# Kernel optimization log

Measured on AMD Instinct MI355X. Metric: run time of the kernel, lower is better.

Reference implementation:

```python
import jax, jax.numpy as jnp
import numpy as np

SEQ_LEN = 4096
IN_DIM = 1024
QVK_DIM = 1024


def setup_inputs() -> dict:
    key = jax.random.key(0)
    kx, kw = jax.random.split(key)
    x = jax.random.normal(kx, (SEQ_LEN, IN_DIM), dtype=jnp.float32)
    # glorot-uniform-ish scale for W: limit = sqrt(6/(fan_in+fan_out))
    limit = np.sqrt(6.0 / (IN_DIM + 3 * QVK_DIM)).astype(np.float32)
    W = jax.random.uniform(kw, (IN_DIM, 3 * QVK_DIM), dtype=jnp.float32,
                           minval=-limit, maxval=limit)
    return {"x": x, "W": W}


def reference(x, W):
    seq_len = x.shape[0]
    qvk = x @ W                                   # [S, 3*D]
    # NOTE: original splits as queries, VALS, keys (vals is the middle chunk)
    queries, vals, keys = jnp.split(qvk, 3, axis=1)
    raw = (queries @ keys.T) / jnp.sqrt(jnp.float32(QVK_DIM))  # [S, S]
    # causal mask: strictly-upper-triangular entries -> -inf (same as the
    # original's scatter of -inf at triu_indices(seq_len, 1))
    causal = jnp.tril(jnp.ones((seq_len, seq_len), dtype=bool))
    raw = jnp.where(causal, raw, -jnp.inf)
    weights = jax.nn.softmax(raw, axis=1)
    return weights @ vals                         # [S, D]
```

## Files before the change

kernel.cpp:

```cpp
#include <hip/hip_runtime.h>

#define SEQ 4096
#define KDIM 1024
#define NQKV 3072
#define BK 32

typedef __bf16 bf16x8 __attribute__((ext_vector_type(8)));
typedef float  f32x4  __attribute__((ext_vector_type(4)));

__device__ __forceinline__ unsigned short f2b(float f) {
    unsigned int u = __float_as_uint(f);
    u += 0x7FFFu + ((u >> 16) & 1u);
    return (unsigned short)(u >> 16);
}
__device__ __forceinline__ float b2f(unsigned short h) {
    return __uint_as_float(((unsigned int)h) << 16);
}

__device__ __forceinline__ void gld_lds16(const unsigned short* g, unsigned short* l) {
    __builtin_amdgcn_global_load_lds(
        (const __attribute__((address_space(1))) void*)g,
        (__attribute__((address_space(3))) void*)l, 16, 0, 0);
}

__device__ __forceinline__ void stage_tiles(
    const unsigned short* Ag, int lda, const unsigned short* Bg, int ldb,
    int k0, unsigned short* sA, unsigned short* sB, int wave, int lane)
{
    #pragma unroll
    for (int i = 0; i < 2; ++i) {
        int c = wave * 128 + i * 64 + lane;
        int row = c >> 2, slot = c & 3;
        int p = slot ^ ((row >> 1) & 3);
        gld_lds16(Ag + row * lda + k0 + p * 8, sA + (wave * 2 + i) * 512);
        gld_lds16(Bg + row * ldb + k0 + p * 8, sB + (wave * 2 + i) * 512);
    }
}

__device__ __forceinline__ const unsigned short* frag_addr(
    const unsigned short* s, int row, int quad)
{
    return s + row * 32 + (quad ^ ((row >> 1) & 3)) * 8;
}

__device__ __forceinline__ void compute_tile(
    const unsigned short* sA, const unsigned short* sB, f32x4 acc[4][4],
    int wm, int wn, int lr, int quad)
{
    bf16x8 af[4], bq[4];
    #pragma unroll
    for (int i = 0; i < 4; ++i)
        af[i] = *(const bf16x8*)frag_addr(sA, wm + 16 * i + lr, quad);
    #pragma unroll
    for (int j = 0; j < 4; ++j)
        bq[j] = *(const bf16x8*)frag_addr(sB, wn + 16 * j + lr, quad);
    #pragma unroll
    for (int i = 0; i < 4; ++i)
        #pragma unroll
        for (int j = 0; j < 4; ++j)
            acc[i][j] = __builtin_amdgcn_mfma_f32_16x16x32_bf16(af[i], bq[j], acc[i][j], 0, 0, 0);
}

__device__ __forceinline__ void mfma_db(
    const unsigned short* Ag, int lda, const unsigned short* Bg, int ldb,
    int kLen, unsigned short* lds, f32x4 acc[4][4])
{
    const int tid  = threadIdx.x;
    const int wave = tid >> 6, lane = tid & 63;
    const int lr   = lane & 15, quad = lane >> 4;
    const int wm   = (wave >> 1) * 64, wn = (wave & 1) * 64;
    unsigned short* sA0 = lds;
    unsigned short* sB0 = lds + 4096;
    unsigned short* sA1 = lds + 8192;
    unsigned short* sB1 = lds + 12288;

    stage_tiles(Ag, lda, Bg, ldb, 0, sA0, sB0, wave, lane);
    int k = BK;
    #pragma unroll 1
    for (; k + BK < kLen; k += 2 * BK) {
        __syncthreads();
        stage_tiles(Ag, lda, Bg, ldb, k, sA1, sB1, wave, lane);
        compute_tile(sA0, sB0, acc, wm, wn, lr, quad);
        __syncthreads();
        stage_tiles(Ag, lda, Bg, ldb, k + BK, sA0, sB0, wave, lane);
        compute_tile(sA1, sB1, acc, wm, wn, lr, quad);
    }
    if (k < kLen) {
        __syncthreads();
        stage_tiles(Ag, lda, Bg, ldb, k, sA1, sB1, wave, lane);
        compute_tile(sA0, sB0, acc, wm, wn, lr, quad);
        __syncthreads();
        compute_tile(sA1, sB1, acc, wm, wn, lr, quad);
    } else {
        __syncthreads();
        compute_tile(sA0, sB0, acc, wm, wn, lr, quad);
    }
}

__device__ __forceinline__ void zero_acc(f32x4 acc[4][4]) {
    const f32x4 z = {0.f, 0.f, 0.f, 0.f};
    #pragma unroll
    for (int i = 0; i < 4; ++i)
        #pragma unroll
        for (int j = 0; j < 4; ++j) acc[i][j] = z;
}

__device__ __forceinline__ void store_rows_bf16(
    f32x4 acc[4][4], unsigned short* Cw, int ld, unsigned short* lw, int lane)
{
    const int lr = lane & 15, quad = lane >> 4;
    #pragma unroll
    for (int i = 0; i < 4; ++i) {
        #pragma unroll
        for (int j = 0; j < 4; ++j)
            #pragma unroll
            for (int r = 0; r < 4; ++r)
                lw[(quad * 4 + r) * 72 + j * 16 + lr] = f2b(acc[i][j][r]);
        #pragma unroll
        for (int t = 0; t < 2; ++t) {
            int chunk = t * 64 + lane;
            int rl = chunk >> 3, c8 = chunk & 7;
            uint4 v = *(const uint4*)(lw + rl * 72 + c8 * 8);
            *(uint4*)(Cw + (16 * i + rl) * ld + c8 * 8) = v;
        }
    }
}

__device__ __forceinline__ void store_cols_bf16(
    f32x4 acc[4][4], unsigned short* Vw, unsigned short* lw, int lane)
{
    const int lr = lane & 15, quad = lane >> 4;
    #pragma unroll
    for (int ip = 0; ip < 2; ++ip) {
        #pragma unroll
        for (int ii = 0; ii < 2; ++ii)
            #pragma unroll
            for (int j = 0; j < 4; ++j)
                #pragma unroll
                for (int r = 0; r < 4; ++r)
                    lw[(j * 16 + lr) * 40 + ii * 16 + quad * 4 + r] = f2b(acc[ip * 2 + ii][j][r]);
        #pragma unroll
        for (int t = 0; t < 4; ++t) {
            int chunk = t * 64 + lane;
            int col = chunk >> 2, c8 = chunk & 3;
            uint4 v = *(const uint4*)(lw + col * 40 + c8 * 8);
            *(uint4*)(Vw + col * SEQ + ip * 32 + c8 * 8) = v;
        }
    }
}

__global__ __launch_bounds__(256) void prep(
    const float* __restrict__ x, unsigned short* __restrict__ Xb,
    const float* __restrict__ W, unsigned short* __restrict__ Wt,
    float4* __restrict__ out, float4* __restrict__ lrow)
{
    __shared__ float tile[32][33];
    const int b = blockIdx.x, tid = threadIdx.x;
    if (b < 4096) {
        int i = (b * 256 + tid) * 4;
        float4 v = *(const float4*)(x + i);
        ushort4 o;
        o.x = f2b(v.x); o.y = f2b(v.y); o.z = f2b(v.z); o.w = f2b(v.w);
        *(ushort4*)(Xb + i) = o;
    } else if (b < 8192) {
        const float4 z = {0.f, 0.f, 0.f, 0.f};
        out[(b - 4096) * 256 + tid] = z;
    } else if (b < 11264) {
        const int bb = b - 8192;
        const int n0 = (bb % 96) * 32, k0 = (bb / 96) * 32;
        const int c = tid & 31, r0 = tid >> 5;
        #pragma unroll
        for (int r = r0; r < 32; r += 8)
            tile[r][c] = W[(k0 + r) * NQKV + n0 + c];
        __syncthreads();
        const int n = tid >> 3, q = tid & 7;
        ushort4 o;
        o.x = f2b(tile[q * 4 + 0][n]);
        o.y = f2b(tile[q * 4 + 1][n]);
        o.z = f2b(tile[q * 4 + 2][n]);
        o.w = f2b(tile[q * 4 + 3][n]);
        *(ushort4*)(Wt + (n0 + n) * KDIM + k0 + q * 4) = o;
    } else {
        const float4 z = {0.f, 0.f, 0.f, 0.f};
        #pragma unroll
        for (int k = 0; k < 4; ++k) lrow[tid * 4 + k] = z;
    }
}

__global__ __launch_bounds__(256) void qvk_gemm(
    const unsigned short* __restrict__ Xb, const unsigned short* __restrict__ Wt,
    unsigned short* __restrict__ Qb, unsigned short* __restrict__ Kb,
    unsigned short* __restrict__ Vt)
{
    __shared__ __align__(16) unsigned short lds[16384];
    const int m0 = blockIdx.y * 128;
    const int n0 = blockIdx.x * 128;
    f32x4 acc[4][4];
    zero_acc(acc);
    mfma_db(Xb + m0 * KDIM, KDIM, Wt + n0 * KDIM, KDIM, KDIM, lds, acc);
    __syncthreads();

    const int lane = threadIdx.x & 63, wave = threadIdx.x >> 6;
    const int wm = (wave >> 1) * 64, wn = (wave & 1) * 64;
    unsigned short* lw = lds + wave * 2560;
    const int region = n0 >> 10;
    const int nloc = n0 & 1023;
    if (region == 0)
        store_rows_bf16(acc, Qb + (m0 + wm) * KDIM + nloc + wn, KDIM, lw, lane);
    else if (region == 2)
        store_rows_bf16(acc, Kb + (m0 + wm) * KDIM + nloc + wn, KDIM, lw, lane);
    else
        store_cols_bf16(acc, Vt + (nloc + wn) * SEQ + m0 + wm, lw, lane);
}

__global__ __launch_bounds__(256) void score_exp_gemm(
    const unsigned short* __restrict__ Qb, const unsigned short* __restrict__ Kb,
    unsigned short* __restrict__ Sb, float* __restrict__ lrow)
{
    __shared__ __align__(16) unsigned short lds[16384];
    const int bm = blockIdx.x, bn = blockIdx.y;
    if (bn > bm) return;
    const int m0 = bm * 128, n0 = bn * 128;

    f32x4 acc[4][4];
    zero_acc(acc);
    mfma_db(Qb + m0 * KDIM, KDIM, Kb + n0 * KDIM, KDIM, KDIM, lds, acc);

    const int lane = threadIdx.x & 63, wave = threadIdx.x >> 6;
    const int lr = lane & 15, quad = lane >> 4;
    const int wm = (wave >> 1) * 64, wn = (wave & 1) * 64;
    #pragma unroll
    for (int i = 0; i < 4; ++i)
        #pragma unroll
        for (int j = 0; j < 4; ++j)
            #pragma unroll
            for (int r = 0; r < 4; ++r) {
                float v = __expf(acc[i][j][r] * 0.03125f);
                if (bm == bn) {
                    int row = wm + 16 * i + quad * 4 + r;
                    int col = wn + 16 * j + lr;
                    if (col > row) v = 0.f;
                }
                acc[i][j][r] = v;
            }
    __syncthreads();
    store_rows_bf16(acc, Sb + (m0 + wm) * SEQ + n0 + wn, SEQ, lds + wave * 2560, lane);
    #pragma unroll
    for (int i = 0; i < 4; ++i)
        #pragma unroll
        for (int r = 0; r < 4; ++r) {
            float s = acc[i][0][r] + acc[i][1][r] + acc[i][2][r] + acc[i][3][r];
            s += __shfl_xor(s, 1, 16);
            s += __shfl_xor(s, 2, 16);
            s += __shfl_xor(s, 4, 16);
            s += __shfl_xor(s, 8, 16);
            if (lr == 0)
                atomicAdd(&lrow[m0 + wm + 16 * i + quad * 4 + r], s);
        }
}

__global__ __launch_bounds__(256) void pv_gemm(
    const unsigned short* __restrict__ Sb, const unsigned short* __restrict__ Vt,
    const float* __restrict__ lrow, float* __restrict__ out)
{
    __shared__ __align__(16) unsigned short lds[16384];
    const int n0 = blockIdx.x * 128;
    const int y = blockIdx.y;
    int m, c;
    if (y < 8)       { m = y;                 c = 0; }
    else if (y < 24) { m = 8 + (y - 8) / 2;   c = (y - 8) % 2; }
    else if (y < 48) { m = 16 + (y - 24) / 3; c = (y - 24) % 3; }
    else             { m = 24 + (y - 48) / 4; c = (y - 48) % 4; }
    const int m0 = m * 128;
    const int kstart = c * 1024;
    const int kend = min((m + 1) * 128, kstart + 1024);
    const int nchunks = (m >> 3) + 1;

    f32x4 acc[4][4];
    zero_acc(acc);
    mfma_db(Sb + m0 * SEQ + kstart, SEQ, Vt + n0 * SEQ + kstart, SEQ,
            kend - kstart, lds, acc);

    const int lane = threadIdx.x & 63, wave = threadIdx.x >> 6;
    const int lr = lane & 15, quad = lane >> 4;
    const int wm = (wave >> 1) * 64, wn = (wave & 1) * 64;
    #pragma unroll
    for (int i = 0; i < 4; ++i) {
        const int rbase = m0 + wm + 16 * i + quad * 4;
        const float4 l4 = *(const float4*)(lrow + rbase);
        float inv[4] = {1.0f / l4.x, 1.0f / l4.y, 1.0f / l4.z, 1.0f / l4.w};
        #pragma unroll
        for (int j = 0; j < 4; ++j) {
            const int col = n0 + wn + 16 * j + lr;
            if (nchunks == 1) {
                #pragma unroll
                for (int r = 0; r < 4; ++r)
                    out[(rbase + r) * KDIM + col] = acc[i][j][r] * inv[r];
            } else {
                #pragma unroll
                for (int r = 0; r < 4; ++r)
                    atomicAdd(&out[(rbase + r) * KDIM + col], acc[i][j][r] * inv[r]);
            }
        }
    }
}

extern "C" void kernel_launch(void* const* d_in, const int* in_sizes, int n_in,
                              void* d_out, int out_size, void* d_ws, size_t ws_size,
                              hipStream_t stream) {
    const float* x = (const float*)d_in[0];
    const float* W = (const float*)d_in[1];
    float* out = (float*)d_out;
    char* ws = (char*)d_ws;

    unsigned short* Xb = (unsigned short*)(ws);
    unsigned short* Wt = (unsigned short*)(ws + 8388608);
    unsigned short* Qb = (unsigned short*)(ws + 14680064);
    unsigned short* Kb = (unsigned short*)(ws + 23068672);
    unsigned short* Vt = (unsigned short*)(ws + 31457280);
    unsigned short* Sb = (unsigned short*)(ws + 39845888);
    float*        lrow = (float*)(ws + 73400320);

    prep          <<<11265, 256, 0, stream>>>(x, Xb, W, Wt, (float4*)out, (float4*)lrow);
    qvk_gemm      <<<dim3(NQKV / 128, SEQ / 128), 256, 0, stream>>>(Xb, Wt, Qb, Kb, Vt);
    score_exp_gemm<<<dim3(SEQ / 128, SEQ / 128), 256, 0, stream>>>(Qb, Kb, Sb, lrow);
    pv_gemm       <<<dim3(KDIM / 128, 80), 256, 0, stream>>>(Sb, Vt, lrow, out);
}
```

Baseline: 203.0 us.

## Replace LDS double-buffered 128x128 GEMM with single-wave 64x64 register-pipelined GEMM

Replaces the shared-memory staged, 4-wave 128x128 tile GEMM core with a single-wave 64x64 tile that loads fragments straight from global memory into registers, software-pipelined four stages deep. The score kernel now launches only the lower-triangular tiles via a triangular index decode instead of early-returning upper blocks, and the PV split-K schedule is remapped to 64-row tiles. This removes LDS staging and barriers but drops cross-wave operand reuse through LDS, raising global/L2 traffic and register pressure.

Result: slower. 332.0 us (+63.6%).

```diff
diff --git a/kernel.cpp b/kernel.cpp
--- a/kernel.cpp
+++ b/kernel.cpp
@@ -3,7 +3,6 @@
 #define SEQ 4096
 #define KDIM 1024
 #define NQKV 3072
-#define BK 32
 
 typedef __bf16 bf16x8 __attribute__((ext_vector_type(8)));
 typedef float  f32x4  __attribute__((ext_vector_type(4)));
@@ -13,88 +12,56 @@
     u += 0x7FFFu + ((u >> 16) & 1u);
     return (unsigned short)(u >> 16);
 }
-__device__ __forceinline__ float b2f(unsigned short h) {
-    return __uint_as_float(((unsigned int)h) << 16);
-}
-
-__device__ __forceinline__ void gld_lds16(const unsigned short* g, unsigned short* l) {
-    __builtin_amdgcn_global_load_lds(
-        (const __attribute__((address_space(1))) void*)g,
-        (__attribute__((address_space(3))) void*)l, 16, 0, 0);
-}
-
-__device__ __forceinline__ void stage_tiles(
-    const unsigned short* Ag, int lda, const unsigned short* Bg, int ldb,
-    int k0, unsigned short* sA, unsigned short* sB, int wave, int lane)
-{
-    #pragma unroll
-    for (int i = 0; i < 2; ++i) {
-        int c = wave * 128 + i * 64 + lane;
-        int row = c >> 2, slot = c & 3;
-        int p = slot ^ ((row >> 1) & 3);
-        gld_lds16(Ag + row * lda + k0 + p * 8, sA + (wave * 2 + i) * 512);
-        gld_lds16(Bg + row * ldb + k0 + p * 8, sB + (wave * 2 + i) * 512);
-    }
-}
-
-__device__ __forceinline__ const unsigned short* frag_addr(
-    const unsigned short* s, int row, int quad)
-{
-    return s + row * 32 + (quad ^ ((row >> 1) & 3)) * 8;
-}
-
-__device__ __forceinline__ void compute_tile(
-    const unsigned short* sA, const unsigned short* sB, f32x4 acc[4][4],
-    int wm, int wn, int lr, int quad)
-{
-    bf16x8 af[4], bq[4];
-    #pragma unroll
-    for (int i = 0; i < 4; ++i)
-        af[i] = *(const bf16x8*)frag_addr(sA, wm + 16 * i + lr, quad);
-    #pragma unroll
-    for (int j = 0; j < 4; ++j)
-        bq[j] = *(const bf16x8*)frag_addr(sB, wn + 16 * j + lr, quad);
-    #pragma unroll
-    for (int i = 0; i < 4; ++i)
-        #pragma unroll
-        for (int j = 0; j < 4; ++j)
-            acc[i][j] = __builtin_amdgcn_mfma_f32_16x16x32_bf16(af[i], bq[j], acc[i][j], 0, 0, 0);
-}
-
-__device__ __forceinline__ void mfma_db(
-    const unsigned short* Ag, int lda, const unsigned short* Bg, int ldb,
-    int kLen, unsigned short* lds, f32x4 acc[4][4])
-{
-    const int tid  = threadIdx.x;
-    const int wave = tid >> 6, lane = tid & 63;
-    const int lr   = lane & 15, quad = lane >> 4;
-    const int wm   = (wave >> 1) * 64, wn = (wave & 1) * 64;
-    unsigned short* sA0 = lds;
-    unsigned short* sB0 = lds + 4096;
-    unsigned short* sA1 = lds + 8192;
-    unsigned short* sB1 = lds + 12288;
-
-    stage_tiles(Ag, lda, Bg, ldb, 0, sA0, sB0, wave, lane);
-    int k = BK;
+
+__device__ __forceinline__ void gemm64_rr(
+    const unsigned short* __restrict__ Ag, int lda,
+    const unsigned short* __restrict__ Bg, int ldb,
+    int kLen, f32x4 acc[4][4])
+{
+    const int lane = threadIdx.x & 63;
+    const int lr = lane & 15, quad = lane >> 4;
+    const unsigned short* ap[4];
+    const unsigned short* bp[4];
+    #pragma unroll
+    for (int i = 0; i < 4; ++i) {
+        ap[i] = Ag + (16 * i + lr) * lda + quad * 8;
+        bp[i] = Bg + (16 * i + lr) * ldb + quad * 8;
+    }
+    bf16x8 Ab[4][4], Bb[4][4];
+    const int niter = kLen >> 5;
+
+#define LOADS(s, off) { \
+    _Pragma("unroll") for (int f = 0; f < 4; ++f) { \
+        Ab[s][f] = *(const bf16x8*)(ap[f] + (off)); \
+        Bb[s][f] = *(const bf16x8*)(bp[f] + (off)); } }
+#define COMP(s) { \
+    _Pragma("unroll") for (int i = 0; i < 4; ++i) \
+    _Pragma("unroll") for (int j = 0; j < 4; ++j) \
+        acc[i][j] = __builtin_amdgcn_mfma_f32_16x16x32_bf16(Ab[s][i], Bb[s][j], acc[i][j], 0, 0, 0); }
+
+    LOADS(0, 0);
+    if (1 < niter) LOADS(1, 32);
+    if (2 < niter) LOADS(2, 64);
+    const int kmain = niter & ~3;
     #pragma unroll 1
-    for (; k + BK < kLen; k += 2 * BK) {
-        __syncthreads();
-        stage_tiles(Ag, lda, Bg, ldb, k, sA1, sB1, wave, lane);
-        compute_tile(sA0, sB0, acc, wm, wn, lr, quad);
-        __syncthreads();
-        stage_tiles(Ag, lda, Bg, ldb, k + BK, sA0, sB0, wave, lane);
-        compute_tile(sA1, sB1, acc, wm, wn, lr, quad);
-    }
-    if (k < kLen) {
-        __syncthreads();
-        stage_tiles(Ag, lda, Bg, ldb, k, sA1, sB1, wave, lane);
-        compute_tile(sA0, sB0, acc, wm, wn, lr, quad);
-        __syncthreads();
-        compute_tile(sA1, sB1, acc, wm, wn, lr, quad);
-    } else {
-        __syncthreads();
-        compute_tile(sA0, sB0, acc, wm, wn, lr, quad);
-    }
+    for (int k = 0; k < kmain; k += 4) {
+        if (k + 3 < niter) LOADS(3, 96);
+        COMP(0);
+        if (k + 4 < niter) LOADS(0, 128);
+        COMP(1);
+        if (k + 5 < niter) LOADS(1, 160);
+        COMP(2);
+        if (k + 6 < niter) LOADS(2, 192);
+        COMP(3);
+        #pragma unroll
+        for (int i = 0; i < 4; ++i) { ap[i] += 128; bp[i] += 128; }
+    }
+    const int rem = niter - kmain;
+    if (rem > 0) COMP(0);
+    if (rem > 1) COMP(1);
+    if (rem > 2) COMP(2);
+#undef LOADS
+#undef COMP
 }
 
 __device__ __forceinline__ void zero_acc(f32x4 acc[4][4]) {
@@ -187,48 +154,48 @@
     }
 }
 
-__global__ __launch_bounds__(256) void qvk_gemm(
+__global__ __launch_bounds__(64, 2) void qvk_gemm(
     const unsigned short* __restrict__ Xb, const unsigned short* __restrict__ Wt,
     unsigned short* __restrict__ Qb, unsigned short* __restrict__ Kb,
     unsigned short* __restrict__ Vt)
 {
-    __shared__ __align__(16) unsigned short lds[16384];
-    const int m0 = blockIdx.y * 128;
-    const int n0 = blockIdx.x * 128;
+    __shared__ __align__(16) unsigned short lw[2560];
+    const int m0 = blockIdx.y * 64;
+    const int n0 = blockIdx.x * 64;
     f32x4 acc[4][4];
     zero_acc(acc);
-    mfma_db(Xb + m0 * KDIM, KDIM, Wt + n0 * KDIM, KDIM, KDIM, lds, acc);
-    __syncthreads();
-
-    const int lane = threadIdx.x & 63, wave = threadIdx.x >> 6;
-    const int wm = (wave >> 1) * 64, wn = (wave & 1) * 64;
-    unsigned short* lw = lds + wave * 2560;
+    gemm64_rr(Xb + m0 * KDIM, KDIM, Wt + n0 * KDIM, KDIM, KDIM, acc);
+
+    const int lane = threadIdx.x & 63;
     const int region = n0 >> 10;
     const int nloc = n0 & 1023;
     if (region == 0)
-        store_rows_bf16(acc, Qb + (m0 + wm) * KDIM + nloc + wn, KDIM, lw, lane);
+        store_rows_bf16(acc, Qb + m0 * KDIM + nloc, KDIM, lw, lane);
     else if (region == 2)
-        store_rows_bf16(acc, Kb + (m0 + wm) * KDIM + nloc + wn, KDIM, lw, lane);
+        store_rows_bf16(acc, Kb + m0 * KDIM + nloc, KDIM, lw, lane);
     else
-        store_cols_bf16(acc, Vt + (nloc + wn) * SEQ + m0 + wm, lw, lane);
-}
-
-__global__ __launch_bounds__(256) void score_exp_gemm(
+        store_cols_bf16(acc, Vt + nloc * SEQ + m0, lw, lane);
+}
+
+__global__ __launch_bounds__(64, 2) void score_exp_gemm(
     const unsigned short* __restrict__ Qb, const unsigned short* __restrict__ Kb,
     unsigned short* __restrict__ Sb, float* __restrict__ lrow)
 {
-    __shared__ __align__(16) unsigned short lds[16384];
-    const int bm = blockIdx.x, bn = blockIdx.y;
-    if (bn > bm) return;
-    const int m0 = bm * 128, n0 = bn * 128;
+    __shared__ __align__(16) unsigned short lw[2560];
+    const int b = blockIdx.x;
+    int mi = (int)((sqrtf(8.f * (float)b + 1.f) - 1.f) * 0.5f);
+    while ((mi + 1) * (mi + 2) / 2 <= b) ++mi;
+    while (mi * (mi + 1) / 2 > b) --mi;
+    const int bn = b - mi * (mi + 1) / 2;
+    const int m0 = mi * 64, n0 = bn * 64;
 
     f32x4 acc[4][4];
     zero_acc(acc);
-    mfma_db(Qb + m0 * KDIM, KDIM, Kb + n0 * KDIM, KDIM, KDIM, lds, acc);
-
-    const int lane = threadIdx.x & 63, wave = threadIdx.x >> 6;
-    const int lr = lane & 15, quad = lane >> 4;
-    const int wm = (wave >> 1) * 64, wn = (wave & 1) * 64;
+    gemm64_rr(Qb + m0 * KDIM, KDIM, Kb + n0 * KDIM, KDIM, KDIM, acc);
+
+    const int lane = threadIdx.x & 63;
+    const int lr = lane & 15, quad = lane >> 4;
+    const bool diag = (bn == mi);
     #pragma unroll
     for (int i = 0; i < 4; ++i)
         #pragma unroll
@@ -236,15 +203,14 @@
             #pragma unroll
             for (int r = 0; r < 4; ++r) {
                 float v = __expf(acc[i][j][r] * 0.03125f);
-                if (bm == bn) {
-                    int row = wm + 16 * i + quad * 4 + r;
-                    int col = wn + 16 * j + lr;
+                if (diag) {
+                    int row = 16 * i + quad * 4 + r;
+                    int col = 16 * j + lr;
                     if (col > row) v = 0.f;
                 }
                 acc[i][j][r] = v;
             }
-    __syncthreads();
-    store_rows_bf16(acc, Sb + (m0 + wm) * SEQ + n0 + wn, SEQ, lds + wave * 2560, lane);
+    store_rows_bf16(acc, Sb + m0 * SEQ + n0, SEQ, lw, lane);
     #pragma unroll
     for (int i = 0; i < 4; ++i)
         #pragma unroll
@@ -255,44 +221,44 @@
             s += __shfl_xor(s, 4, 16);
             s += __shfl_xor(s, 8, 16);
             if (lr == 0)
-                atomicAdd(&lrow[m0 + wm + 16 * i + quad * 4 + r], s);
-        }
-}
-
-__global__ __launch_bounds__(256) void pv_gemm(
+                atomicAdd(&lrow[m0 + 16 * i + quad * 4 + r], s);
+        }
+}
+
+__global__ __launch_bounds__(64, 2) void pv_gemm(
     const unsigned short* __restrict__ Sb, const unsigned short* __restrict__ Vt,
     const float* __restrict__ lrow, float* __restrict__ out)
 {
-    __shared__ __align__(16) unsigned short lds[16384];
-    const int n0 = blockIdx.x * 128;
+    const int n0 = blockIdx.x * 64;
     const int y = blockIdx.y;
-    int m, c;
-    if (y < 8)       { m = y;                 c = 0; }
-    else if (y < 24) { m = 8 + (y - 8) / 2;   c = (y - 8) % 2; }
-    else if (y < 48) { m = 16 + (y - 24) / 3; c = (y - 24) % 3; }
-    else             { m = 24 + (y - 48) / 4; c = (y - 48) % 4; }
-    const int m0 = m * 128;
+    int g, base;
+    if (y < 16)      { g = 0; base = 0; }
+    else if (y < 48) { g = 1; base = 16; }
+    else if (y < 96) { g = 2; base = 48; }
+    else             { g = 3; base = 96; }
+    const int yy = y - base;
+    const int mi = 16 * g + yy / (g + 1);
+    const int c = yy % (g + 1);
+    const int m0 = mi * 64;
     const int kstart = c * 1024;
-    const int kend = min((m + 1) * 128, kstart + 1024);
-    const int nchunks = (m >> 3) + 1;
+    const int kend = min(m0 + 64, kstart + 1024);
 
     f32x4 acc[4][4];
     zero_acc(acc);
-    mfma_db(Sb + m0 * SEQ + kstart, SEQ, Vt + n0 * SEQ + kstart, SEQ,
-            kend - kstart, lds, acc);
-
-    const int lane = threadIdx.x & 63, wave = threadIdx.x >> 6;
-    const int lr = lane & 15, quad = lane >> 4;
-    const int wm = (wave >> 1) * 64, wn = (wave & 1) * 64;
+    gemm64_rr(Sb + m0 * SEQ + kstart, SEQ, Vt + n0 * SEQ + kstart, SEQ,
+              kend - kstart, acc);
+
+    const int lane = threadIdx.x & 63;
+    const int lr = lane & 15, quad = lane >> 4;
     #pragma unroll
     for (int i = 0; i < 4; ++i) {
-        const int rbase = m0 + wm + 16 * i + quad * 4;
+        const int rbase = m0 + 16 * i + quad * 4;
         const float4 l4 = *(const float4*)(lrow + rbase);
         float inv[4] = {1.0f / l4.x, 1.0f / l4.y, 1.0f / l4.z, 1.0f / l4.w};
         #pragma unroll
         for (int j = 0; j < 4; ++j) {
-            const int col = n0 + wn + 16 * j + lr;
-            if (nchunks == 1) {
+            const int col = n0 + 16 * j + lr;
+            if (g == 0) {
                 #pragma unroll
                 for (int r = 0; r < 4; ++r)
                     out[(rbase + r) * KDIM + col] = acc[i][j][r] * inv[r];
@@ -322,7 +288,7 @@
     float*        lrow = (float*)(ws + 73400320);
 
     prep          <<<11265, 256, 0, stream>>>(x, Xb, W, Wt, (float4*)out, (float4*)lrow);
-    qvk_gemm      <<<dim3(NQKV / 128, SEQ / 128), 256, 0, stream>>>(Xb, Wt, Qb, Kb, Vt);
-    score_exp_gemm<<<dim3(SEQ / 128, SEQ / 128), 256, 0, stream>>>(Qb, Kb, Sb, lrow);
-    pv_gemm       <<<dim3(KDIM / 128, 80), 256, 0, stream>>>(Sb, Vt, lrow, out);
-}
+    qvk_gemm      <<<dim3(NQKV / 64, SEQ / 64), 64, 0, stream>>>(Xb, Wt, Qb, Kb, Vt);
+    score_exp_gemm<<<2080, 64, 0, stream>>>(Qb, Kb, Sb, lrow);
+    pv_gemm       <<<dim3(KDIM / 64, 160), 64, 0, stream>>>(Sb, Vt, lrow, out);
+}
```

## Fuse QKV, score and PV GEMMs into one persistent dependency-scheduled kernel

Applied to the files above, without the earlier changes.

Replaces the three separate GEMM launches with a single persistent kernel. Blocks pull tiles from an atomic work counter and wait on per-row-block completion counters (Q/K done, V done, score rows done) using acquire/release atomics and sleep-spin. This lets score and PV tiles start as soon as their inputs are ready, overlapping stage tails and removing launch gaps. The cost is spin-waiting, extra fences, and reliance on all workgroups being co-resident. The counters sit in an unused corner of the score buffer, which only works because that region is never written or read.

Measured after the change: 548.1 us. 2.7x slower.

```diff
diff --git a/kernel.cpp b/kernel.cpp
--- a/kernel.cpp
+++ b/kernel.cpp
@@ -5,6 +5,11 @@
 #define NQKV 3072
 #define BK 32
 
+#define N_QVK   768
+#define N_SCORE 528
+#define N_PV    640
+#define N_TOTAL (N_QVK + N_SCORE + N_PV)
+
 typedef __bf16 bf16x8 __attribute__((ext_vector_type(8)));
 typedef float  f32x4  __attribute__((ext_vector_type(4)));
 
@@ -12,9 +17,6 @@
     unsigned int u = __float_as_uint(f);
     u += 0x7FFFu + ((u >> 16) & 1u);
     return (unsigned short)(u >> 16);
-}
-__device__ __forceinline__ float b2f(unsigned short h) {
-    return __uint_as_float(((unsigned int)h) << 16);
 }
 
 __device__ __forceinline__ void gld_lds16(const unsigned short* g, unsigned short* l) {
@@ -152,7 +154,7 @@
 __global__ __launch_bounds__(256) void prep(
     const float* __restrict__ x, unsigned short* __restrict__ Xb,
     const float* __restrict__ W, unsigned short* __restrict__ Wt,
-    float4* __restrict__ out, float4* __restrict__ lrow)
+    float4* __restrict__ out, float4* __restrict__ lrow, int* __restrict__ ctr)
 {
     __shared__ float tile[32][33];
     const int b = blockIdx.x, tid = threadIdx.x;
@@ -184,122 +186,158 @@
         const float4 z = {0.f, 0.f, 0.f, 0.f};
         #pragma unroll
         for (int k = 0; k < 4; ++k) lrow[tid * 4 + k] = z;
-    }
-}
-
-__global__ __launch_bounds__(256) void qvk_gemm(
+        if (tid < 128) ctr[tid] = 0;
+    }
+}
+
+__global__ __launch_bounds__(256, 3) void attn(
     const unsigned short* __restrict__ Xb, const unsigned short* __restrict__ Wt,
     unsigned short* __restrict__ Qb, unsigned short* __restrict__ Kb,
-    unsigned short* __restrict__ Vt)
+    unsigned short* __restrict__ Vt, unsigned short* __restrict__ Sb,
+    float* __restrict__ lrow, float* __restrict__ out, int* __restrict__ ctr)
 {
     __shared__ __align__(16) unsigned short lds[16384];
-    const int m0 = blockIdx.y * 128;
-    const int n0 = blockIdx.x * 128;
-    f32x4 acc[4][4];
-    zero_acc(acc);
-    mfma_db(Xb + m0 * KDIM, KDIM, Wt + n0 * KDIM, KDIM, KDIM, lds, acc);
-    __syncthreads();
-
-    const int lane = threadIdx.x & 63, wave = threadIdx.x >> 6;
-    const int wm = (wave >> 1) * 64, wn = (wave & 1) * 64;
-    unsigned short* lw = lds + wave * 2560;
-    const int region = n0 >> 10;
-    const int nloc = n0 & 1023;
-    if (region == 0)
-        store_rows_bf16(acc, Qb + (m0 + wm) * KDIM + nloc + wn, KDIM, lw, lane);
-    else if (region == 2)
-        store_rows_bf16(acc, Kb + (m0 + wm) * KDIM + nloc + wn, KDIM, lw, lane);
-    else
-        store_cols_bf16(acc, Vt + (nloc + wn) * SEQ + m0 + wm, lw, lane);
-}
-
-__global__ __launch_bounds__(256) void score_exp_gemm(
-    const unsigned short* __restrict__ Qb, const unsigned short* __restrict__ Kb,
-    unsigned short* __restrict__ Sb, float* __restrict__ lrow)
-{
-    __shared__ __align__(16) unsigned short lds[16384];
-    const int bm = blockIdx.x, bn = blockIdx.y;
-    if (bn > bm) return;
-    const int m0 = bm * 128, n0 = bn * 128;
-
-    f32x4 acc[4][4];
-    zero_acc(acc);
-    mfma_db(Qb + m0 * KDIM, KDIM, Kb + n0 * KDIM, KDIM, KDIM, lds, acc);
-
-    const int lane = threadIdx.x & 63, wave = threadIdx.x >> 6;
+    __shared__ int t_sh;
+    int* work  = ctr;
+    int* vcnt  = ctr + 1;
+    int* qdone = ctr + 8;
+    int* kdone = ctr + 40;
+    int* sdone = ctr + 72;
+
+    const int tid  = threadIdx.x;
+    const int wave = tid >> 6, lane = tid & 63;
     const int lr = lane & 15, quad = lane >> 4;
     const int wm = (wave >> 1) * 64, wn = (wave & 1) * 64;
-    #pragma unroll
-    for (int i = 0; i < 4; ++i)
-        #pragma unroll
-        for (int j = 0; j < 4; ++j)
-            #pragma unroll
-            for (int r = 0; r < 4; ++r) {
-                float v = __expf(acc[i][j][r] * 0.03125f);
-                if (bm == bn) {
-                    int row = wm + 16 * i + quad * 4 + r;
-                    int col = wn + 16 * j + lr;
-                    if (col > row) v = 0.f;
+
+    while (true) {
+        __syncthreads();
+        if (tid == 0)
+            t_sh = __hip_atomic_fetch_add(work, 1, __ATOMIC_RELAXED,
+                                          __HIP_MEMORY_SCOPE_AGENT);
+        __syncthreads();
+        const int t = t_sh;
+        if (t >= N_TOTAL) return;
+
+        if (t < N_QVK) {
+            int m, nb;
+            if (t < 512) { m = t >> 4; int r = t & 15; nb = (r < 8) ? r : r + 8; }
+            else         { int u = t - 512; m = u >> 3; nb = 8 + (u & 7); }
+            const int m0 = m * 128, n0 = nb * 128;
+            f32x4 acc[4][4];
+            zero_acc(acc);
+            mfma_db(Xb + m0 * KDIM, KDIM, Wt + n0 * KDIM, KDIM, KDIM, lds, acc);
+            __syncthreads();
+            unsigned short* lw = lds + wave * 2560;
+            const int region = n0 >> 10;
+            const int nloc = n0 & 1023;
+            if (region == 0)
+                store_rows_bf16(acc, Qb + (m0 + wm) * KDIM + nloc + wn, KDIM, lw, lane);
+            else if (region == 2)
+                store_rows_bf16(acc, Kb + (m0 + wm) * KDIM + nloc + wn, KDIM, lw, lane);
+            else
+                store_cols_bf16(acc, Vt + (nloc + wn) * SEQ + m0 + wm, lw, lane);
+            __threadfence();
+            __syncthreads();
+            if (tid == 0) {
+                int* d = (region == 0) ? &qdone[m] : (region == 2) ? &kdone[m] : vcnt;
+                __hip_atomic_fetch_add(d, 1, __ATOMIC_RELEASE, __HIP_MEMORY_SCOPE_AGENT);
+            }
+        } else if (t < N_QVK + N_SCORE) {
+            const int b = t - N_QVK;
+            int bm = (int)((sqrtf(8.f * (float)b + 1.f) - 1.f) * 0.5f);
+            while ((bm + 1) * (bm + 2) / 2 <= b) ++bm;
+            while (bm * (bm + 1) / 2 > b) --bm;
+            const int bn = b - bm * (bm + 1) / 2;
+            const int m0 = bm * 128, n0 = bn * 128;
+            if (tid == 0) {
+                while (__hip_atomic_load(&qdone[bm], __ATOMIC_ACQUIRE,
+                                         __HIP_MEMORY_SCOPE_AGENT) < 8 ||
+                       __hip_atomic_load(&kdone[bn], __ATOMIC_ACQUIRE,
+                                         __HIP_MEMORY_SCOPE_AGENT) < 8)
+                    __builtin_amdgcn_s_sleep(2);
+            }
+            __syncthreads();
+
+            f32x4 acc[4][4];
+            zero_acc(acc);
+            mfma_db(Qb + m0 * KDIM, KDIM, Kb + n0 * KDIM, KDIM, KDIM, lds, acc);
+            #pragma unroll
+            for (int i = 0; i < 4; ++i)
+                #pragma unroll
+                for (int j = 0; j < 4; ++j)
+                    #pragma unroll
+                    for (int r = 0; r < 4; ++r) {
+                        float v = __expf(acc[i][j][r] * 0.03125f);
+                        if (bm == bn) {
+                            int row = wm + 16 * i + quad * 4 + r;
+                            int col = wn + 16 * j + lr;
+                            if (col > row) v = 0.f;
+                        }
+                        acc[i][j][r] = v;
+                    }
+            __syncthreads();
+            store_rows_bf16(acc, Sb + (m0 + wm) * SEQ + n0 + wn, SEQ, lds + wave * 2560, lane);
+            #pragma unroll
+            for (int i = 0; i < 4; ++i)
+                #pragma unroll
+                for (int r = 0; r < 4; ++r) {
+                    float s = acc[i][0][r] + acc[i][1][r] + acc[i][2][r] + acc[i][3][r];
+                    s += __shfl_xor(s, 1, 16);
+                    s += __shfl_xor(s, 2, 16);
+                    s += __shfl_xor(s, 4, 16);
+                    s += __shfl_xor(s, 8, 16);
+                    if (lr == 0)
+                        atomicAdd(&lrow[m0 + wm + 16 * i + quad * 4 + r], s);
                 }
-                acc[i][j][r] = v;
+            __threadfence();
+            __syncthreads();
+            if (tid == 0)
+                __hip_atomic_fetch_add(&sdone[bm], 1, __ATOMIC_RELEASE,
+                                       __HIP_MEMORY_SCOPE_AGENT);
+        } else {
+            const int p = t - N_QVK - N_SCORE;
+            const int n0 = (p & 7) * 128;
+            const int y = p >> 3;
+            int m, c;
+            if (y < 8)       { m = y;                 c = 0; }
+            else if (y < 24) { m = 8 + (y - 8) / 2;   c = (y - 8) % 2; }
+            else if (y < 48) { m = 16 + (y - 24) / 3; c = (y - 24) % 3; }
+            else             { m = 24 + (y - 48) / 4; c = (y - 48) % 4; }
+            const int m0 = m * 128;
+            const int kstart = c * 1024;
+            const int kend = min((m + 1) * 128, kstart + 1024);
+            const int nchunks = (m >> 3) + 1;
+            if (tid == 0) {
+                while (__hip_atomic_load(&sdone[m], __ATOMIC_ACQUIRE,
+                                         __HIP_MEMORY_SCOPE_AGENT) < m + 1 ||
+                       __hip_atomic_load(vcnt, __ATOMIC_ACQUIRE,
+                                         __HIP_MEMORY_SCOPE_AGENT) < 256)
+                    __builtin_amdgcn_s_sleep(2);
             }
-    __syncthreads();
-    store_rows_bf16(acc, Sb + (m0 + wm) * SEQ + n0 + wn, SEQ, lds + wave * 2560, lane);
-    #pragma unroll
-    for (int i = 0; i < 4; ++i)
-        #pragma unroll
-        for (int r = 0; r < 4; ++r) {
-            float s = acc[i][0][r] + acc[i][1][r] + acc[i][2][r] + acc[i][3][r];
-            s += __shfl_xor(s, 1, 16);
-            s += __shfl_xor(s, 2, 16);
-            s += __shfl_xor(s, 4, 16);
-            s += __shfl_xor(s, 8, 16);
-            if (lr == 0)
-                atomicAdd(&lrow[m0 + wm + 16 * i + quad * 4 + r], s);
-        }
-}
-
-__global__ __launch_bounds__(256) void pv_gemm(
-    const unsigned short* __restrict__ Sb, const unsigned short* __restrict__ Vt,
-    const float* __restrict__ lrow, float* __restrict__ out)
-{
-    __shared__ __align__(16) unsigned short lds[16384];
-    const int n0 = blockIdx.x * 128;
-    const int y = blockIdx.y;
-    int m, c;
-    if (y < 8)       { m = y;                 c = 0; }
-    else if (y < 24) { m = 8 + (y - 8) / 2;   c = (y - 8) % 2; }
-    else if (y < 48) { m = 16 + (y - 24) / 3; c = (y - 24) % 3; }
-    else             { m = 24 + (y - 48) / 4; c = (y - 48) % 4; }
-    const int m0 = m * 128;
-    const int kstart = c * 1024;
-    const int kend = min((m + 1) * 128, kstart + 1024);
-    const int nchunks = (m >> 3) + 1;
-
-    f32x4 acc[4][4];
-    zero_acc(acc);
-    mfma_db(Sb + m0 * SEQ + kstart, SEQ, Vt + n0 * SEQ + kstart, SEQ,
-            kend - kstart, lds, acc);
-
-    const int lane = threadIdx.x & 63, wave = threadIdx.x >> 6;
-    const int lr = lane & 15, quad = lane >> 4;
-    const int wm = (wave >> 1) * 64, wn = (wave & 1) * 64;
-    #pragma unroll
-    for (int i = 0; i < 4; ++i) {
-        const int rbase = m0 + wm + 16 * i + quad * 4;
-        const float4 l4 = *(const float4*)(lrow + rbase);
-        float inv[4] = {1.0f / l4.x, 1.0f / l4.y, 1.0f / l4.z, 1.0f / l4.w};
-        #pragma unroll
-        for (int j = 0; j < 4; ++j) {
-            const int col = n0 + wn + 16 * j + lr;
-            if (nchunks == 1) {
+            __syncthreads();
+
+            f32x4 acc[4][4];
+            zero_acc(acc);
+            mfma_db(Sb + m0 * SEQ + kstart, SEQ, Vt + n0 * SEQ + kstart, SEQ,
+                    kend - kstart, lds, acc);
+            #pragma unroll
+            for (int i = 0; i < 4; ++i) {
+                const int rbase = m0 + wm + 16 * i + quad * 4;
+                const float4 l4 = *(const float4*)(lrow + rbase);
+                float inv[4] = {1.0f / l4.x, 1.0f / l4.y, 1.0f / l4.z, 1.0f / l4.w};
                 #pragma unroll
-                for (int r = 0; r < 4; ++r)
-                    out[(rbase + r) * KDIM + col] = acc[i][j][r] * inv[r];
-            } else {
-                #pragma unroll
-                for (int r = 0; r < 4; ++r)
-                    atomicAdd(&out[(rbase + r) * KDIM + col], acc[i][j][r] * inv[r]);
+                for (int j = 0; j < 4; ++j) {
+                    const int col = n0 + wn + 16 * j + lr;
+                    if (nchunks == 1) {
+                        #pragma unroll
+                        for (int r = 0; r < 4; ++r)
+                            out[(rbase + r) * KDIM + col] = acc[i][j][r] * inv[r];
+                    } else {
+                        #pragma unroll
+                        for (int r = 0; r < 4; ++r)
+                            atomicAdd(&out[(rbase + r) * KDIM + col], acc[i][j][r] * inv[r]);
+                    }
+                }
             }
         }
     }
@@ -320,9 +358,8 @@
     unsigned short* Vt = (unsigned short*)(ws + 31457280);
     unsigned short* Sb = (unsigned short*)(ws + 39845888);
     float*        lrow = (float*)(ws + 73400320);
-
-    prep          <<<11265, 256, 0, stream>>>(x, Xb, W, Wt, (float4*)out, (float4*)lrow);
-    qvk_gemm      <<<dim3(NQKV / 128, SEQ / 128), 256, 0, stream>>>(Xb, Wt, Qb, Kb, Vt);
-    score_exp_gemm<<<dim3(SEQ / 128, SEQ / 128), 256, 0, stream>>>(Qb, Kb, Sb, lrow);
-    pv_gemm       <<<dim3(KDIM / 128, 80), 256, 0, stream>>>(Sb, Vt, lrow, out);
-}
+    int*           ctr = (int*)(ws + 39845888 + 3840 * 2);
+
+    prep<<<11265, 256, 0, stream>>>(x, Xb, W, Wt, (float4*)out, (float4*)lrow, ctr);
+    attn<<<768, 256, 0, stream>>>(Xb, Wt, Qb, Kb, Vt, Sb, lrow, out, ctr);
+}
```
